# Kernel optimization log

Measured on AMD Instinct MI355X. Metric: run time of the kernel, lower is better.

The kernel has to match this reference:

```python
import jax, jax.numpy as jnp
import numpy as np
from jax.ops import segment_sum, segment_max

N_NODES = 50000
N_EDGES = 800000
B = 1024            # number of graphs
NODE_DIM = 21
ESM_DIM = 480
TAB_DIM = 7
H = 128             # hidden_dim
LSTM_H = H // 2     # 64 per direction
NEG_SLOPE = 0.2
BN_EPS = 1e-5


def setup_inputs() -> dict:
    key = jax.random.key(0)
    ks = iter(jax.random.split(key, 48))
    r = lambda shape, s=0.05: (s * jax.random.normal(next(ks), shape)).astype(jnp.float32)
    inp = {
        'x': jax.random.normal(next(ks), (N_NODES, NODE_DIM), dtype=jnp.float32),
        'edge_index': jax.random.randint(next(ks), (2, N_EDGES), 0, N_NODES, dtype=jnp.int64),
        'batch': jnp.sort(jax.random.randint(next(ks), (N_NODES,), 0, B, dtype=jnp.int64)),
        'esm_emb': jax.random.normal(next(ks), (B, ESM_DIM), dtype=jnp.float32),
        'tab_feats': jax.random.normal(next(ks), (B, TAB_DIM), dtype=jnp.float32),
        # GATConv 1 (heads=1)
        'gat1_W': r((H, NODE_DIM)), 'gat1_asrc': r((H,)), 'gat1_adst': r((H,)), 'gat1_b': r((H,)),
        # GATConv 2
        'gat2_W': r((H, H)), 'gat2_asrc': r((H,)), 'gat2_adst': r((H,)), 'gat2_b': r((H,)),
        # Bidirectional LSTM (seq_len=1, so a single cell step per direction)
        'lstm_Wih_f': r((4 * LSTM_H, ESM_DIM)), 'lstm_Whh_f': r((4 * LSTM_H, LSTM_H)),
        'lstm_bih_f': r((4 * LSTM_H,)), 'lstm_bhh_f': r((4 * LSTM_H,)),
        'lstm_Wih_r': r((4 * LSTM_H, ESM_DIM)), 'lstm_Whh_r': r((4 * LSTM_H, LSTM_H)),
        'lstm_bih_r': r((4 * LSTM_H,)), 'lstm_bhh_r': r((4 * LSTM_H,)),
        # tabular net
        'tab_W': r((64, TAB_DIM)), 'tab_b': r((64,)), 'tab_bn_g': jnp.ones((64,), jnp.float32), 'tab_bn_b': jnp.zeros((64,), jnp.float32),
        # fusion head
        'fus1_W': r((256, 320)), 'fus1_b': r((256,)), 'fus_bn_g': jnp.ones((256,), jnp.float32), 'fus_bn_b': jnp.zeros((256,), jnp.float32),
        'fus2_W': r((128, 256)), 'fus2_b': r((128,)),
        'fus3_W': r((1, 128)), 'fus3_b': r((1,)),
    }
    return inp


def _gat(h_in, src, dst, W, a_src, a_dst, bias):
    # PyG GATConv, heads=1, concat=True, self-loops already appended.
    h = h_in @ W.T                                  # [N, H]
    alpha_s = h @ a_src                             # [N]
    alpha_d = h @ a_dst                             # [N]
    e = jax.nn.leaky_relu(alpha_s[src] + alpha_d[dst], NEG_SLOPE)  # [E]
    m = segment_max(e, dst, num_segments=N_NODES)   # stable softmax per target
    ex = jnp.exp(e - m[dst])
    den = segment_sum(ex, dst, num_segments=N_NODES)
    coef = ex / (den[dst] + 1e-16)
    out = segment_sum(coef[:, None] * h[src], dst, num_segments=N_NODES)
    return out + bias


def _bn(x, g, b):
    # BatchNorm1d in training mode: biased batch statistics
    mu = jnp.mean(x, axis=0)
    var = jnp.var(x, axis=0)
    return (x - mu) * jax.lax.rsqrt(var + BN_EPS) * g + b


def _lstm_step(x, Wih, Whh, bih, bhh):
    # single step with zero initial (h, c); Whh term vanishes but kept for fidelity
    g = x @ Wih.T + bih + jnp.zeros((x.shape[0], Whh.shape[1]), x.dtype) @ Whh.T + bhh
    i, f, gg, o = jnp.split(g, 4, axis=1)           # PyTorch gate order i,f,g,o
    c = jax.nn.sigmoid(i) * jnp.tanh(gg)
    return jax.nn.sigmoid(o) * jnp.tanh(c)


def reference(x, edge_index, batch, esm_emb, tab_feats,
              gat1_W, gat1_asrc, gat1_adst, gat1_b,
              gat2_W, gat2_asrc, gat2_adst, gat2_b,
              lstm_Wih_f, lstm_Whh_f, lstm_bih_f, lstm_bhh_f,
              lstm_Wih_r, lstm_Whh_r, lstm_bih_r, lstm_bhh_r,
              tab_W, tab_b, tab_bn_g, tab_bn_b,
              fus1_W, fus1_b, fus_bn_g, fus_bn_b,
              fus2_W, fus2_b, fus3_W, fus3_b):
    sl = jnp.arange(N_NODES, dtype=edge_index.dtype)
    src = jnp.concatenate([edge_index[0], sl])      # add_self_loops=True default
    dst = jnp.concatenate([edge_index[1], sl])

    h1 = jax.nn.relu(_gat(x, src, dst, gat1_W, gat1_asrc, gat1_adst, gat1_b))
    h2 = jax.nn.relu(_gat(h1, src, dst, gat2_W, gat2_asrc, gat2_adst, gat2_b))

    counts = segment_sum(jnp.ones((N_NODES,), h2.dtype), batch, num_segments=B)
    graph_embed = segment_sum(h2, batch, num_segments=B) / jnp.maximum(counts, 1.0)[:, None]

    # bilstm over seq_len=1: output at last (only) step = concat(fwd, bwd)
    h_f = _lstm_step(esm_emb, lstm_Wih_f, lstm_Whh_f, lstm_bih_f, lstm_bhh_f)
    h_r = _lstm_step(esm_emb, lstm_Wih_r, lstm_Whh_r, lstm_bih_r, lstm_bhh_r)
    seq_embed = jnp.concatenate([h_f, h_r], axis=1)  # [B, 128]

    tab_embed = jax.nn.relu(_bn(tab_feats @ tab_W.T + tab_b, tab_bn_g, tab_bn_b))

    z = jnp.concatenate([graph_embed, seq_embed, tab_embed], axis=1)  # [B, 320]
    z = jax.nn.relu(_bn(z @ fus1_W.T + fus1_b, fus_bn_g, fus_bn_b))   # dropout: identity (eval)
    z = jax.nn.relu(z @ fus2_W.T + fus2_b)
    return z @ fus3_W.T + fus3_b                     # [B, 1]
```

## Files before the change

### kernel.cpp

```cpp
#include <hip/hip_runtime.h>
#include <hip/hip_bf16.h>

#define N_NODES 50000
#define N_PAD   50048
#define N_EDGES 800000
#define E_TOT   850000
#define NB      1024
#define ESM_DIM 480
#define HD      128
#define NBUCK   196
#define CAP     5120
#define EPB     3321
#define SC_BLK  256
#define CVT_BLK 256
#define BND_BLK 196
#define WC_BLK  16
#define TAB_BLK 4
#define G1B     782
#define LSTM_B  48
#define LG      384
#define AGG_GRID 12500
#define NL_BLK  512

typedef short short8 __attribute__((ext_vector_type(8)));
typedef unsigned short ushort8 __attribute__((ext_vector_type(8)));
typedef float f32x4 __attribute__((ext_vector_type(4)));

__device__ __forceinline__ float bf2f(unsigned int u) {
    union { unsigned int i; float f; } c; c.i = u << 16; return c.f;
}
__device__ __forceinline__ unsigned short f2bf(float f) {
    union { float f; unsigned int i; } c; c.f = f;
    unsigned int i = c.i;
    return (unsigned short)((i + 0x7FFFu + ((i >> 16) & 1u)) >> 16);
}
__device__ __forceinline__ void split2(float v, unsigned short& h, unsigned short& l) {
    h = f2bf(v);
    l = f2bf(v - bf2f(h));
}


__device__ void dev_scatter(const int* __restrict__ ei, int* __restrict__ gcur,
                            int* __restrict__ pairs, int blk) {
    __shared__ int hist[NBUCK];
    int t = threadIdx.x;
    for (int u = t; u < NBUCK; u += 256) hist[u] = 0;
    __syncthreads();
    int e0 = blk * EPB;
    int e1 = (e0 + EPB < E_TOT) ? e0 + EPB : E_TOT;
    for (int e = e0 + t; e < e1; e += 256) {
        int d = (e < N_EDGES) ? ei[N_EDGES + e] : (e - N_EDGES);
        atomicAdd(&hist[d >> 8], 1);
    }
    __syncthreads();
    for (int u = t; u < NBUCK; u += 256) {
        int c = hist[u];
        hist[u] = (c > 0) ? atomicAdd(&gcur[u], c) : 0;
    }
    __syncthreads();
    for (int e = e0 + t; e < e1; e += 256) {
        int s, d;
        if (e < N_EDGES) { s = ei[e]; d = ei[N_EDGES + e]; }
        else             { s = d = e - N_EDGES; }
        int bu = d >> 8;
        int pos = atomicAdd(&hist[bu], 1);
        pairs[bu * CAP + pos] = s | ((d & 255) << 16);
    }
}

__device__ void dev_cvt(const float* __restrict__ esm,
                        const float* __restrict__ Wf,
                        const float* __restrict__ Wr,
                        const float* __restrict__ W1,
                        unsigned short* __restrict__ esm_h, unsigned short* __restrict__ esm_l,
                        unsigned short* __restrict__ wg_h,  unsigned short* __restrict__ wg_l,
                        unsigned short* __restrict__ w1h,   unsigned short* __restrict__ w1l,
                        int blk) {
    int tid = blk * 256 + threadIdx.x;
    for (int u = tid; u < NB * 120; u += CVT_BLK * 256) {
        float4 v = ((const float4*)esm)[u];
        ushort4 h, l;
        split2(v.x, h.x, l.x); split2(v.y, h.y, l.y);
        split2(v.z, h.z, l.z); split2(v.w, h.w, l.w);
        ((ushort4*)esm_h)[u] = h; ((ushort4*)esm_l)[u] = l;
    }
    for (int u = tid; u < LG * 120; u += CVT_BLK * 256) {
        int n = u / 120, kk = u - n * 120;
        int rr = (n >= 192) ? n - 192 : n;
        const float* Ws = (n >= 192) ? Wr : Wf;
        int srow = (rr < 64) ? rr : rr + 64;
        float4 v = *(const float4*)&Ws[(size_t)srow * 480 + kk * 4];
        ushort4 h, l;
        split2(v.x, h.x, l.x); split2(v.y, h.y, l.y);
        split2(v.z, h.z, l.z); split2(v.w, h.w, l.w);
        ((ushort4*)wg_h)[u] = h; ((ushort4*)wg_l)[u] = l;
    }
    for (int u = tid; u < 128 * 32; u += CVT_BLK * 256) {
        int f = u >> 5, k = u & 31;
        float v = (k < 21) ? W1[f * 21 + k] : 0.f;
        unsigned short h, l;
        split2(v, h, l);
        w1h[u] = h; w1l[u] = l;
    }
}

__device__ void dev_tab4(const float* __restrict__ tf, const float* __restrict__ W,
                         const float* __restrict__ bias, const float* __restrict__ g,
                         const float* __restrict__ b, float* __restrict__ z, int blk) {
    __shared__ float ssum[16][16];
    __shared__ float ssq[16][16];
    int t = threadIdx.x;
    int rg = t >> 4, jl = t & 15;
    int j = blk * 16 + jl;
    float Wj[7];
#pragma unroll
    for (int k = 0; k < 7; ++k) Wj[k] = W[j * 7 + k];
    float bj = bias[j];
    float s = 0.f, q = 0.f;
    for (int rr = 0; rr < 64; ++rr) {
        int row = rg * 64 + rr;
        const float* xp = &tf[(size_t)row * 7];
        float a = bj;
#pragma unroll
        for (int k = 0; k < 7; ++k) a += xp[k] * Wj[k];
        s += a; q += a * a;
    }
    ssum[rg][jl] = s; ssq[rg][jl] = q;
    __syncthreads();
    for (int off = 8; off; off >>= 1) {
        if (rg < off) { ssum[rg][jl] += ssum[rg + off][jl]; ssq[rg][jl] += ssq[rg + off][jl]; }
        __syncthreads();
    }
    float mu = ssum[0][jl] * (1.f / 1024.f);
    float var = ssq[0][jl] * (1.f / 1024.f) - mu * mu;
    float sc = rsqrtf(var + 1e-5f) * g[j];
    float sh = b[j] - mu * sc;
    for (int rr = 0; rr < 64; ++rr) {
        int row = rg * 64 + rr;
        const float* xp = &tf[(size_t)row * 7];
        float a = bj;
#pragma unroll
        for (int k = 0; k < 7; ++k) a += xp[k] * Wj[k];
        z[(size_t)row * 320 + 256 + j] = fmaxf(a * sc + sh, 0.f);
    }
}

__global__ __launch_bounds__(256) void megaA(
        const int* __restrict__ ei, int* __restrict__ gcur, int* __restrict__ pairs,
        const float* __restrict__ esm, const float* __restrict__ Wih_f,
        const float* __restrict__ Wih_r, const float* __restrict__ gat1_W,
        unsigned short* __restrict__ esm_h, unsigned short* __restrict__ esm_l,
        unsigned short* __restrict__ wg_h,  unsigned short* __restrict__ wg_l,
        unsigned short* __restrict__ w1h,   unsigned short* __restrict__ w1l,
        const int* __restrict__ batch, int* __restrict__ gstart,
        const float* __restrict__ W2, unsigned short* __restrict__ Wb,
        const float* __restrict__ tf, const float* __restrict__ tab_W,
        const float* __restrict__ tab_b, const float* __restrict__ tab_g,
        const float* __restrict__ tab_bb, float* __restrict__ z) {
    int b = blockIdx.x, t = threadIdx.x;
    if (b < SC_BLK) {
        dev_scatter(ei, gcur, pairs, b);
    } else if (b < SC_BLK + CVT_BLK) {
        dev_cvt(esm, Wih_f, Wih_r, gat1_W, esm_h, esm_l, wg_h, wg_l, w1h, w1l, b - SC_BLK);
    } else if (b < SC_BLK + CVT_BLK + BND_BLK) {
        int i = (b - (SC_BLK + CVT_BLK)) * 256 + t;
        if (i >= N_NODES) return;
        int bb = batch[i];
        int bp = (i == 0) ? -1 : batch[i - 1];
        for (int g = bp + 1; g <= bb; ++g) gstart[g] = i;
        if (i == N_NODES - 1)
            for (int g = bb + 1; g <= NB; ++g) gstart[g] = N_NODES;
    } else if (b < SC_BLK + CVT_BLK + BND_BLK + WC_BLK) {
        int i = (b - (SC_BLK + CVT_BLK + BND_BLK)) * 256 + t;
        if (i >= 128 * 32) return;
        float4 v = ((const float4*)W2)[i];
        ((ushort4*)Wb)[i] = make_ushort4(f2bf(v.x), f2bf(v.y), f2bf(v.z), f2bf(v.w));
    } else {
        dev_tab4(tf, tab_W, tab_b, tab_g, tab_bb, z,
                 b - (SC_BLK + CVT_BLK + BND_BLK + WC_BLK));
    }
}


__device__ __forceinline__ float sigmoidf_(float x) { return 1.f / (1.f + __expf(-x)); }

__device__ void dev_gat1_mfma(const float* __restrict__ X,
                              const unsigned short* __restrict__ w1h,
                              const unsigned short* __restrict__ w1l,
                              const float* __restrict__ asrc, const float* __restrict__ adst,
                              unsigned short* __restrict__ out,
                              float* __restrict__ alpha_s, float* __restrict__ alpha_d,
                              int blk) {
    int t = threadIdx.x;
    int wid = t >> 6, L = t & 63, quad = L >> 4, lo = L & 15;
    int m0 = blk * 64 + wid * 16;
    int row = m0 + lo;
    const float* xr = X + (size_t)row * 21;
    int kbase = quad * 8;
    bool valid = row < N_NODES;
    float xv[8];
#pragma unroll
    for (int j = 0; j < 8; ++j) {
        int k = kbase + j;
        xv[j] = (valid && k < 21) ? xr[k] : 0.f;
    }
    short8 ah, al;
#pragma unroll
    for (int j = 0; j < 8; ++j) {
        unsigned short h, l;
        split2(xv[j], h, l);
        ah[j] = (short)h; al[j] = (short)l;
    }
    float as_p[4] = {0.f, 0.f, 0.f, 0.f};
    float ad_p[4] = {0.f, 0.f, 0.f, 0.f};
#pragma unroll
    for (int ft = 0; ft < 8; ++ft) {
        short8 bh = *(const short8*)&w1h[(ft * 16 + lo) * 32 + kbase];
        short8 bl = *(const short8*)&w1l[(ft * 16 + lo) * 32 + kbase];
        f32x4 acc = {0.f, 0.f, 0.f, 0.f};
        acc = __builtin_amdgcn_mfma_f32_16x16x32_bf16(ah, bh, acc, 0, 0, 0);
        acc = __builtin_amdgcn_mfma_f32_16x16x32_bf16(al, bh, acc, 0, 0, 0);
        acc = __builtin_amdgcn_mfma_f32_16x16x32_bf16(ah, bl, acc, 0, 0, 0);
        float asv = asrc[ft * 16 + lo];
        float adv = adst[ft * 16 + lo];
#pragma unroll
        for (int r = 0; r < 4; ++r) {
            int m = m0 + quad * 4 + r;
            out[(size_t)m * HD + ft * 16 + lo] = f2bf(acc[r]);
            as_p[r] += acc[r] * asv;
            ad_p[r] += acc[r] * adv;
        }
    }
#pragma unroll
    for (int off = 1; off < 16; off <<= 1) {
#pragma unroll
        for (int r = 0; r < 4; ++r) {
            as_p[r] += __shfl_xor(as_p[r], off);
            ad_p[r] += __shfl_xor(ad_p[r], off);
        }
    }
    if (lo == 0) {
#pragma unroll
        for (int r = 0; r < 4; ++r) {
            int m = m0 + quad * 4 + r;
            if (m < N_NODES) { alpha_s[m] = as_p[r]; alpha_d[m] = ad_p[r]; }
        }
    }
}

__device__ void dev_lstm_mfma(const unsigned short* __restrict__ Ah,
                              const unsigned short* __restrict__ Al,
                              const unsigned short* __restrict__ Bh,
                              const unsigned short* __restrict__ Bl,
                              float* __restrict__ G, int blk) {
    int t = threadIdx.x;
    int wid = t >> 6, L = t & 63, quad = L >> 4, lo = L & 15;
    int nt = blk % 3, mt = blk / 3;
    int m0 = mt * 64 + wid * 16;
    int n0 = nt * 128;
    f32x4 accs[8];
#pragma unroll
    for (int ft = 0; ft < 8; ++ft) accs[ft] = (f32x4){0.f, 0.f, 0.f, 0.f};
    const unsigned short* arh = Ah + (size_t)(m0 + lo) * ESM_DIM;
    const unsigned short* arl = Al + (size_t)(m0 + lo) * ESM_DIM;
    for (int k0 = 0; k0 < ESM_DIM; k0 += 32) {
        short8 ah = *(const short8*)&arh[k0 + quad * 8];
        short8 al = *(const short8*)&arl[k0 + quad * 8];
#pragma unroll
        for (int ft = 0; ft < 8; ++ft) {
            size_t boff = (size_t)(n0 + ft * 16 + lo) * ESM_DIM + k0 + quad * 8;
            short8 bh = *(const short8*)&Bh[boff];
            short8 bl = *(const short8*)&Bl[boff];
            accs[ft] = __builtin_amdgcn_mfma_f32_16x16x32_bf16(ah, bh, accs[ft], 0, 0, 0);
            accs[ft] = __builtin_amdgcn_mfma_f32_16x16x32_bf16(al, bh, accs[ft], 0, 0, 0);
            accs[ft] = __builtin_amdgcn_mfma_f32_16x16x32_bf16(ah, bl, accs[ft], 0, 0, 0);
        }
    }
#pragma unroll
    for (int ft = 0; ft < 8; ++ft) {
#pragma unroll
        for (int r = 0; r < 4; ++r)
            G[(size_t)(m0 + quad * 4 + r) * LG + n0 + ft * 16 + lo] = accs[ft][r];
    }
}

__global__ __launch_bounds__(256) void megaB(
        const int* __restrict__ gcur, const int* __restrict__ pairs,
        int* __restrict__ row_beg, int* __restrict__ row_end, int* __restrict__ csr_src,
        const float* __restrict__ x,
        const unsigned short* __restrict__ w1h, const unsigned short* __restrict__ w1l,
        const float* __restrict__ gat1_as, const float* __restrict__ gat1_ad,
        unsigned short* __restrict__ h0, float* __restrict__ alpha_s, float* __restrict__ alpha_d,
        const unsigned short* __restrict__ esm_h, const unsigned short* __restrict__ esm_l,
        const unsigned short* __restrict__ wg_h,  const unsigned short* __restrict__ wg_l,
        float* __restrict__ g_lstm) {
    int b = blockIdx.x, t = threadIdx.x;
    if (b < NBUCK) {
        __shared__ int dc[256];
        __shared__ int wt[4];
        __shared__ int cur[256];
        int rs = b * CAP;
        int re = rs + gcur[b];
        dc[t] = 0;
        __syncthreads();
        for (int i = rs + t; i < re; i += 256) atomicAdd(&dc[pairs[i] >> 16], 1);
        __syncthreads();
        int v = dc[t];
        int lane = t & 63, wid = t >> 6;
        int sc = v;
#pragma unroll
        for (int off = 1; off < 64; off <<= 1) {
            int n = __shfl_up(sc, off);
            if (lane >= off) sc += n;
        }
        if (lane == 63) wt[wid] = sc;
        __syncthreads();
        int pref = 0;
        for (int ww = 0; ww < wid; ++ww) pref += wt[ww];
        int beg = rs + pref + sc - v;
        int node = b * 256 + t;
        if (node < N_NODES) { row_beg[node] = beg; row_end[node] = beg + v; }
        cur[t] = beg;
        __syncthreads();
        for (int i = rs + t; i < re; i += 256) {
            int pk = pairs[i];
            int pos = atomicAdd(&cur[pk >> 16], 1);
            csr_src[pos] = pk & 0xFFFF;
        }
    } else if (b < NBUCK + LSTM_B) {
        dev_lstm_mfma(esm_h, esm_l, wg_h, wg_l, g_lstm, b - NBUCK);
    } else {
        dev_gat1_mfma(x, w1h, w1l, gat1_as, gat1_ad, h0, alpha_s, alpha_d,
                      b - (NBUCK + LSTM_B));
    }
}


__global__ __launch_bounds__(256) void gemm_mfma(const unsigned short* __restrict__ A,
                                                 const unsigned short* __restrict__ Wb,
                                                 const float* __restrict__ asrc,
                                                 const float* __restrict__ adst,
                                                 unsigned short* __restrict__ out,
                                                 float* __restrict__ alpha_s,
                                                 float* __restrict__ alpha_d, int M) {
    __shared__ unsigned short Wlds[128 * 136];
    int t = threadIdx.x;
    for (int u = t; u < 128 * 16; u += 256) {
        int row = u >> 4, seg = u & 15;
        *(ushort8*)&Wlds[row * 136 + seg * 8] = *(const ushort8*)&Wb[row * 128 + seg * 8];
    }
    __syncthreads();
    int wid = t >> 6, L = t & 63;
    int quad = L >> 4, lo = L & 15;
    int m0 = blockIdx.x * 64 + wid * 16;
    short8 afrag[4];
#pragma unroll
    for (int ch = 0; ch < 4; ++ch)
        afrag[ch] = *(const short8*)&A[(size_t)(m0 + lo) * HD + ch * 32 + quad * 8];
    float as_p[4] = {0.f, 0.f, 0.f, 0.f};
    float ad_p[4] = {0.f, 0.f, 0.f, 0.f};
#pragma unroll
    for (int ft = 0; ft < 8; ++ft) {
        f32x4 acc = {0.f, 0.f, 0.f, 0.f};
#pragma unroll
        for (int ch = 0; ch < 4; ++ch) {
            short8 b = *(const short8*)&Wlds[(ft * 16 + lo) * 136 + ch * 32 + quad * 8];
            acc = __builtin_amdgcn_mfma_f32_16x16x32_bf16(afrag[ch], b, acc, 0, 0, 0);
        }
        float asv = asrc[ft * 16 + lo];
        float adv = adst[ft * 16 + lo];
#pragma unroll
        for (int r = 0; r < 4; ++r) {
            int m = m0 + quad * 4 + r;
            if (m < M) out[(size_t)m * HD + ft * 16 + lo] = f2bf(acc[r]);
            as_p[r] += acc[r] * asv;
            ad_p[r] += acc[r] * adv;
        }
    }
#pragma unroll
    for (int off = 1; off < 16; off <<= 1) {
#pragma unroll
        for (int r = 0; r < 4; ++r) {
            as_p[r] += __shfl_xor(as_p[r], off);
            ad_p[r] += __shfl_xor(ad_p[r], off);
        }
    }
    if (lo == 0) {
#pragma unroll
        for (int r = 0; r < 4; ++r) {
            int m = m0 + quad * 4 + r;
            if (m < M) { alpha_s[m] = as_p[r]; alpha_d[m] = ad_p[r]; }
        }
    }
}


__global__ void gat_spmm(const unsigned short* __restrict__ h, const int* __restrict__ row_beg,
                         const int* __restrict__ row_end, const int* __restrict__ csr_src,
                         const float* __restrict__ alpha_s, const float* __restrict__ alpha_d,
                         const float* __restrict__ bias, unsigned short* __restrict__ outp,
                         const float* __restrict__ g_lstm,
                         const float* __restrict__ bihf, const float* __restrict__ bhhf,
                         const float* __restrict__ bihr, const float* __restrict__ bhhr,
                         float* __restrict__ z) {
    if (blockIdx.x >= AGG_GRID) {
        int idx = (blockIdx.x - AGG_GRID) * 256 + threadIdx.x;
        int bb = idx >> 7, jj = idx & 127;
        int dir = jj >> 6, j = jj & 63;
        const float* gb = g_lstm + (size_t)bb * LG + dir * 192;
        const float* bi = dir ? bihr : bihf;
        const float* bh = dir ? bhhr : bhhf;
        float gi = gb[j]        + bi[j]        + bh[j];
        float gg = gb[64 + j]   + bi[128 + j]  + bh[128 + j];
        float go = gb[128 + j]  + bi[192 + j]  + bh[192 + j];
        float c = sigmoidf_(gi) * tanhf(gg);
        z[(size_t)bb * 320 + 128 + jj] = sigmoidf_(go) * tanhf(c);
        return;
    }
    int w = (int)((blockIdx.x * (size_t)blockDim.x + threadIdx.x) >> 6);
    int lane = threadIdx.x & 63;
    if (w >= N_NODES) return;
    int grp = lane >> 4, l16 = lane & 15;
    int rs = row_beg[w], re = row_end[w];
    int deg = re - rs;
    float ad = alpha_d[w];
    float acc[8] = {0.f, 0.f, 0.f, 0.f, 0.f, 0.f, 0.f, 0.f};
    if (deg <= 64) {
        int s_reg = 0;
        float e = -1e30f;
        if (lane < deg) {
            s_reg = csr_src[rs + lane];
            float t0 = alpha_s[s_reg] + ad;
            e = (t0 > 0.f) ? t0 : 0.2f * t0;
        }
        float m = e;
#pragma unroll
        for (int off = 32; off; off >>= 1) m = fmaxf(m, __shfl_xor(m, off));
        float ex = (lane < deg) ? __expf(e - m) : 0.f;
        float den = ex;
#pragma unroll
        for (int off = 32; off; off >>= 1) den += __shfl_xor(den, off);
        float coef = ex / (den + 1e-16f);
        int i = rs + grp;
        for (; i + 4 < re; i += 8) {
            int idx = i - rs;
            float c0 = __shfl(coef, idx);
            int   s0 = __shfl(s_reg, idx);
            float c1 = __shfl(coef, idx + 4);
            int   s1 = __shfl(s_reg, idx + 4);
            ushort8 h0 = *(const ushort8*)&h[(size_t)s0 * HD + l16 * 8];
            ushort8 h1 = *(const ushort8*)&h[(size_t)s1 * HD + l16 * 8];
#pragma unroll
            for (int j = 0; j < 8; ++j) acc[j] += c0 * bf2f(h0[j]);
#pragma unroll
            for (int j = 0; j < 8; ++j) acc[j] += c1 * bf2f(h1[j]);
        }
        if (i < re) {
            int idx = i - rs;
            float c0 = __shfl(coef, idx);
            int   s0 = __shfl(s_reg, idx);
            ushort8 h0 = *(const ushort8*)&h[(size_t)s0 * HD + l16 * 8];
#pragma unroll
            for (int j = 0; j < 8; ++j) acc[j] += c0 * bf2f(h0[j]);
        }
    } else {
        float m = -1e30f;
        for (int i = rs + lane; i < re; i += 64) {
            int s = csr_src[i];
            float t0 = alpha_s[s] + ad;
            t0 = (t0 > 0.f) ? t0 : 0.2f * t0;
            m = fmaxf(m, t0);
        }
#pragma unroll
        for (int off = 32; off; off >>= 1) m = fmaxf(m, __shfl_xor(m, off));
        float den = 0.f;
        for (int i = rs + lane; i < re; i += 64) {
            int s = csr_src[i];
            float t0 = alpha_s[s] + ad;
            t0 = (t0 > 0.f) ? t0 : 0.2f * t0;
            den += __expf(t0 - m);
        }
#pragma unroll
        for (int off = 32; off; off >>= 1) den += __shfl_xor(den, off);
        float inv = 1.f / (den + 1e-16f);
        for (int i = rs + grp; i < re; i += 4) {
            int s = csr_src[i];
            float t0 = alpha_s[s] + ad;
            t0 = (t0 > 0.f) ? t0 : 0.2f * t0;
            float c = __expf(t0 - m) * inv;
            ushort8 hv = *(const ushort8*)&h[(size_t)s * HD + l16 * 8];
#pragma unroll
            for (int j = 0; j < 8; ++j) acc[j] += c * bf2f(hv[j]);
        }
    }
#pragma unroll
    for (int j = 0; j < 8; ++j) {
        acc[j] += __shfl_xor(acc[j], 16);
        acc[j] += __shfl_xor(acc[j], 32);
    }
    int f0 = l16 * 8 + grp * 2;
    float2 bv = *(const float2*)&bias[f0];
    float vx = fmaxf(acc[grp * 2]     + bv.x, 0.f);
    float vy = fmaxf(acc[grp * 2 + 1] + bv.y, 0.f);
    unsigned int pv = (unsigned int)f2bf(vx) | ((unsigned int)f2bf(vy) << 16);
    *(unsigned int*)&outp[(size_t)w * HD + f0] = pv;
}


__global__ void pool_kernel(const unsigned short* __restrict__ h, const int* __restrict__ start,
                            float* __restrict__ z) {
    int w = (int)((blockIdx.x * (size_t)blockDim.x + threadIdx.x) >> 6);
    int lane = threadIdx.x & 63;
    if (w >= NB) return;
    int grp = lane >> 4, l16 = lane & 15;
    int s0 = start[w], s1 = start[w + 1];
    float acc[8] = {0.f, 0.f, 0.f, 0.f, 0.f, 0.f, 0.f, 0.f};
    int n = s0 + grp;
    for (; n + 4 < s1; n += 8) {
        ushort8 a = *(const ushort8*)&h[(size_t)n * HD + l16 * 8];
        ushort8 b = *(const ushort8*)&h[(size_t)(n + 4) * HD + l16 * 8];
#pragma unroll
        for (int j = 0; j < 8; ++j) acc[j] += bf2f(a[j]);
#pragma unroll
        for (int j = 0; j < 8; ++j) acc[j] += bf2f(b[j]);
    }
    if (n < s1) {
        ushort8 a = *(const ushort8*)&h[(size_t)n * HD + l16 * 8];
#pragma unroll
        for (int j = 0; j < 8; ++j) acc[j] += bf2f(a[j]);
    }
#pragma unroll
    for (int j = 0; j < 8; ++j) {
        acc[j] += __shfl_xor(acc[j], 16);
        acc[j] += __shfl_xor(acc[j], 32);
    }
    float inv = 1.f / fmaxf((float)(s1 - s0), 1.f);
    int f0 = l16 * 8 + grp * 2;
    *(float2*)&z[(size_t)w * 320 + f0] =
        make_float2(acc[grp * 2] * inv, acc[grp * 2 + 1] * inv);
}


__global__ __launch_bounds__(256) void fus1_stats(const float* __restrict__ X,
                                                  const float* __restrict__ W1,
                                                  float* __restrict__ out,
                                                  float* __restrict__ colsum,
                                                  float* __restrict__ colsq) {
    __shared__ float Xs[16][33];
    __shared__ float Ws[64][33];
    __shared__ float cs[4][64];
    __shared__ float cq[4][64];
    int t = threadIdx.x;
    int r0 = blockIdx.x * 16;
    int fb = blockIdx.y * 64;
    const float* W = W1 + (size_t)fb * 320;
    int f = t & 63, rsub = t >> 6;
    float acc0 = 0.f, acc1 = 0.f, acc2 = 0.f, acc3 = 0.f;
    for (int kc = 0; kc < 320; kc += 32) {
        {
            int idx = t * 2, xr = idx >> 5, xk = idx & 31;
            const float2 v = *(const float2*)&X[(size_t)(r0 + xr) * 320 + kc + xk];
            Xs[xr][xk] = v.x; Xs[xr][xk + 1] = v.y;
        }
        {
            int wf = t >> 2, wk = (t & 3) * 8;
            const float4* p = (const float4*)&W[(size_t)wf * 320 + kc + wk];
            float4 a = p[0], b = p[1];
            Ws[wf][wk] = a.x; Ws[wf][wk + 1] = a.y; Ws[wf][wk + 2] = a.z; Ws[wf][wk + 3] = a.w;
            Ws[wf][wk + 4] = b.x; Ws[wf][wk + 5] = b.y; Ws[wf][wk + 6] = b.z; Ws[wf][wk + 7] = b.w;
        }
        __syncthreads();
#pragma unroll
        for (int k = 0; k < 32; ++k) {
            float w = Ws[f][k];
            acc0 += Xs[rsub][k] * w;
            acc1 += Xs[rsub + 4][k] * w;
            acc2 += Xs[rsub + 8][k] * w;
            acc3 += Xs[rsub + 12][k] * w;
        }
        __syncthreads();
    }
    out[(size_t)(r0 + rsub) * 256 + fb + f] = acc0;
    out[(size_t)(r0 + rsub + 4) * 256 + fb + f] = acc1;
    out[(size_t)(r0 + rsub + 8) * 256 + fb + f] = acc2;
    out[(size_t)(r0 + rsub + 12) * 256 + fb + f] = acc3;
    cs[rsub][f] = acc0 + acc1 + acc2 + acc3;
    cq[rsub][f] = acc0 * acc0 + acc1 * acc1 + acc2 * acc2 + acc3 * acc3;
    __syncthreads();
    if (rsub == 0) {
        atomicAdd(&colsum[fb + f], cs[0][f] + cs[1][f] + cs[2][f] + cs[3][f]);
        atomicAdd(&colsq[fb + f],  cq[0][f] + cq[1][f] + cq[2][f] + cq[3][f]);
    }
}


__global__ __launch_bounds__(256) void fus2_final(const float* __restrict__ z1pre,
                                                  const float* __restrict__ colsum,
                                                  const float* __restrict__ colsq,
                                                  const float* __restrict__ fus_g,
                                                  const float* __restrict__ fus_bb,
                                                  const float* __restrict__ W2,
                                                  const float* __restrict__ b2,
                                                  const float* __restrict__ W3,
                                                  const float* __restrict__ b3,
                                                  float* __restrict__ out) {
    __shared__ float Xs[16][33];
    __shared__ float Ws[128][33];
    __shared__ float rowsum[16];
    __shared__ float sc_[256], sh_[256];
    int t = threadIdx.x;
    {
        float mu = colsum[t] * (1.f / 1024.f);
        float var = colsq[t] * (1.f / 1024.f) - mu * mu;
        float s = rsqrtf(var + 1e-5f) * fus_g[t];
        sc_[t] = s;
        sh_[t] = fus_bb[t] - mu * s;
    }
    __syncthreads();
    int r0 = blockIdx.x * 16;
    int f = t & 127, rh = t >> 7;
    float acc[8] = {0.f, 0.f, 0.f, 0.f, 0.f, 0.f, 0.f, 0.f};
    for (int kc = 0; kc < 256; kc += 32) {
        {
            int idx = t * 2, xr = idx >> 5, xk = idx & 31;
            float2 v = *(const float2*)&z1pre[(size_t)(r0 + xr) * 256 + kc + xk];
            Xs[xr][xk]     = fmaxf(v.x * sc_[kc + xk]     + sh_[kc + xk], 0.f);
            Xs[xr][xk + 1] = fmaxf(v.y * sc_[kc + xk + 1] + sh_[kc + xk + 1], 0.f);
        }
#pragma unroll
        for (int i = 0; i < 4; ++i) {
            int id2 = t + 256 * i;
            int wf = id2 >> 3, wk = (id2 & 7) * 4;
            *(float4*)&Ws[wf][wk] = *(const float4*)&W2[(size_t)wf * 256 + kc + wk];
        }
        __syncthreads();
#pragma unroll
        for (int k = 0; k < 32; ++k) {
            float w = Ws[f][k];
#pragma unroll
            for (int r = 0; r < 8; ++r) acc[r] += Xs[rh * 8 + r][k] * w;
        }
        __syncthreads();
    }
    float bv = b2[f], wv = W3[f];
    if (t < 16) rowsum[t] = 0.f;
    __syncthreads();
#pragma unroll
    for (int r = 0; r < 8; ++r) {
        float v = fmaxf(acc[r] + bv, 0.f) * wv;
#pragma unroll
        for (int off = 32; off; off >>= 1) v += __shfl_xor(v, off);
        if ((t & 63) == 0) atomicAdd(&rowsum[rh * 8 + r], v);
    }
    __syncthreads();
    if (t < 16) out[r0 + t] = rowsum[t] + b3[0];
}


extern "C" void kernel_launch(void* const* d_in, const int* in_sizes, int n_in,
                              void* d_out, int out_size, void* d_ws, size_t ws_size,
                              hipStream_t stream) {
    const float* x        = (const float*)d_in[0];
    const int*   ei       = (const int*)d_in[1];
    const int*   batch    = (const int*)d_in[2];
    const float* esm      = (const float*)d_in[3];
    const float* tabf     = (const float*)d_in[4];
    const float* gat1_W   = (const float*)d_in[5];
    const float* gat1_as  = (const float*)d_in[6];
    const float* gat1_ad  = (const float*)d_in[7];
    const float* gat1_b   = (const float*)d_in[8];
    const float* gat2_W   = (const float*)d_in[9];
    const float* gat2_as  = (const float*)d_in[10];
    const float* gat2_ad  = (const float*)d_in[11];
    const float* gat2_b   = (const float*)d_in[12];
    const float* Wih_f    = (const float*)d_in[13];
    const float* bih_f    = (const float*)d_in[15];
    const float* bhh_f    = (const float*)d_in[16];
    const float* Wih_r    = (const float*)d_in[17];
    const float* bih_r    = (const float*)d_in[19];
    const float* bhh_r    = (const float*)d_in[20];
    const float* tab_W    = (const float*)d_in[21];
    const float* tab_b    = (const float*)d_in[22];
    const float* tab_g    = (const float*)d_in[23];
    const float* tab_bb   = (const float*)d_in[24];
    const float* fus1_W   = (const float*)d_in[25];
    const float* fus_g    = (const float*)d_in[27];
    const float* fus_bb   = (const float*)d_in[28];
    const float* fus2_W   = (const float*)d_in[29];
    const float* fus2_b   = (const float*)d_in[30];
    const float* fus3_W   = (const float*)d_in[31];
    const float* fus3_b   = (const float*)d_in[32];
    float* out = (float*)d_out;

    char* ws = (char*)d_ws;
    size_t off = 0;
    auto alloc = [&](size_t bytes) -> char* {
        char* p = ws + off;
        off += (bytes + 255) & ~(size_t)255;
        return p;
    };
    unsigned short* h0_bf = (unsigned short*)alloc((size_t)N_PAD * HD * 2);
    unsigned short* hA_bf = (unsigned short*)alloc((size_t)N_PAD * HD * 2);
    unsigned short* h2_bf = (unsigned short*)alloc((size_t)N_PAD * HD * 2);
    unsigned short* h_act = (unsigned short*)alloc((size_t)N_NODES * HD * 2);
    float* alpha_s = (float*)alloc((size_t)N_NODES * 4);
    float* alpha_d = (float*)alloc((size_t)N_NODES * 4);
    unsigned short* w2bf = (unsigned short*)alloc((size_t)HD * HD * 2);
    int*   row_beg = (int*)alloc((size_t)N_NODES * 4);
    int*   row_end = (int*)alloc((size_t)N_NODES * 4);
    int*   csr_src = (int*)alloc((size_t)NBUCK * CAP * 4);
    int*   pairs   = (int*)alloc((size_t)NBUCK * CAP * 4);
    int*   gstart  = (int*)alloc((size_t)(NB + 1) * 4);
    float* z1pre   = (float*)alloc((size_t)NB * 256 * 4);
    float* z       = (float*)alloc((size_t)NB * 320 * 4);
    float* g_lstm  = (float*)alloc((size_t)NB * LG * 4);
    unsigned short* esm_h = (unsigned short*)alloc((size_t)NB * ESM_DIM * 2);
    unsigned short* esm_l = (unsigned short*)alloc((size_t)NB * ESM_DIM * 2);
    unsigned short* wg_h  = (unsigned short*)alloc((size_t)LG * ESM_DIM * 2);
    unsigned short* wg_l  = (unsigned short*)alloc((size_t)LG * ESM_DIM * 2);
    unsigned short* w1h   = (unsigned short*)alloc((size_t)128 * 32 * 2);
    unsigned short* w1l   = (unsigned short*)alloc((size_t)128 * 32 * 2);
    int*   gcur    = (int*)alloc((size_t)NBUCK * 4);
    float* colsum  = (float*)alloc((size_t)256 * 4);
    float* colsq   = (float*)alloc((size_t)256 * 4);
    size_t zero_len = (size_t)((char*)colsq + 256 * 4 - (char*)gcur);
    hipMemsetAsync(gcur, 0, zero_len, stream);

    megaA<<<SC_BLK + CVT_BLK + BND_BLK + WC_BLK + TAB_BLK, 256, 0, stream>>>(
        ei, gcur, pairs, esm, Wih_f, Wih_r, gat1_W,
        esm_h, esm_l, wg_h, wg_l, w1h, w1l,
        batch, gstart, gat2_W, w2bf,
        tabf, tab_W, tab_b, tab_g, tab_bb, z);

    megaB<<<NBUCK + LSTM_B + G1B, 256, 0, stream>>>(
        gcur, pairs, row_beg, row_end, csr_src,
        x, w1h, w1l, gat1_as, gat1_ad, h0_bf, alpha_s, alpha_d,
        esm_h, esm_l, wg_h, wg_l, g_lstm);

    gat_spmm<<<AGG_GRID + NL_BLK, 256, 0, stream>>>(h0_bf, row_beg, row_end, csr_src,
                                                    alpha_s, alpha_d, gat1_b, hA_bf,
                                                    g_lstm, bih_f, bhh_f, bih_r, bhh_r, z);

    gemm_mfma<<<N_PAD / 64, 256, 0, stream>>>(hA_bf, w2bf, gat2_as, gat2_ad,
                                              h2_bf, alpha_s, alpha_d, N_NODES);

    gat_spmm<<<AGG_GRID, 256, 0, stream>>>(h2_bf, row_beg, row_end, csr_src,
                                           alpha_s, alpha_d, gat2_b, h_act,
                                           g_lstm, bih_f, bhh_f, bih_r, bhh_r, z);

    pool_kernel<<<(NB + 3) / 4, 256, 0, stream>>>(h_act, gstart, z);

    fus1_stats<<<dim3(64, 4), 256, 0, stream>>>(z, fus1_W, z1pre, colsum, colsq);

    fus2_final<<<64, 256, 0, stream>>>(z1pre, colsum, colsq, fus_g, fus_bb,
                                       fus2_W, fus2_b, fus3_W, fus3_b, out);

    (void)in_sizes; (void)n_in; (void)out_size; (void)ws_size;
}
```

Before: 332.3 us.

## Stage LSTM weights in LDS with finer N tiles and batch bucket pair loads

The LSTM gate GEMM inside megaB now uses 64-wide N tiles, which doubles its block count, and stages the hi/lo weight tiles in shared memory in K chunks of 96 so the four waves share them instead of each reading global memory. The CSR bucket build loops now load four pairs per thread per iteration before doing the LDS atomics, to raise memory-level parallelism. The cost is extra LDS use and barriers in the LSTM blocks, and more LSTM blocks competing with the other roles in the merged kernel.

```diff
diff --git a/kernel.cpp b/kernel.cpp
--- a/kernel.cpp
+++ b/kernel.cpp
@@ -17,7 +17,7 @@
 #define WC_BLK  16
 #define TAB_BLK 4
 #define G1B     782
-#define LSTM_B  48
+#define LSTM_B  96
 #define LG      384
 #define AGG_GRID 12500
 #define NL_BLK  512
@@ -253,31 +253,51 @@
                               const unsigned short* __restrict__ Bh,
                               const unsigned short* __restrict__ Bl,
                               float* __restrict__ G, int blk) {
+    __shared__ unsigned short Bsh[64][104];
+    __shared__ unsigned short Bsl[64][104];
     int t = threadIdx.x;
     int wid = t >> 6, L = t & 63, quad = L >> 4, lo = L & 15;
-    int nt = blk % 3, mt = blk / 3;
+    int nt = blk % 6, mt = blk / 6;
     int m0 = mt * 64 + wid * 16;
-    int n0 = nt * 128;
-    f32x4 accs[8];
-#pragma unroll
-    for (int ft = 0; ft < 8; ++ft) accs[ft] = (f32x4){0.f, 0.f, 0.f, 0.f};
+    int n0 = nt * 64;
+    f32x4 accs[4];
+#pragma unroll
+    for (int ft = 0; ft < 4; ++ft) accs[ft] = (f32x4){0.f, 0.f, 0.f, 0.f};
     const unsigned short* arh = Ah + (size_t)(m0 + lo) * ESM_DIM;
     const unsigned short* arl = Al + (size_t)(m0 + lo) * ESM_DIM;
-    for (int k0 = 0; k0 < ESM_DIM; k0 += 32) {
-        short8 ah = *(const short8*)&arh[k0 + quad * 8];
-        short8 al = *(const short8*)&arl[k0 + quad * 8];
-#pragma unroll
-        for (int ft = 0; ft < 8; ++ft) {
-            size_t boff = (size_t)(n0 + ft * 16 + lo) * ESM_DIM + k0 + quad * 8;
-            short8 bh = *(const short8*)&Bh[boff];
-            short8 bl = *(const short8*)&Bl[boff];
-            accs[ft] = __builtin_amdgcn_mfma_f32_16x16x32_bf16(ah, bh, accs[ft], 0, 0, 0);
-            accs[ft] = __builtin_amdgcn_mfma_f32_16x16x32_bf16(al, bh, accs[ft], 0, 0, 0);
-            accs[ft] = __builtin_amdgcn_mfma_f32_16x16x32_bf16(ah, bl, accs[ft], 0, 0, 0);
-        }
-    }
-#pragma unroll
-    for (int ft = 0; ft < 8; ++ft) {
+    for (int c = 0; c < 5; ++c) {
+        int k0c = c * 96;
+        short8 ah[3], al[3];
+#pragma unroll
+        for (int ks = 0; ks < 3; ++ks) {
+            ah[ks] = *(const short8*)&arh[k0c + ks * 32 + quad * 8];
+            al[ks] = *(const short8*)&arl[k0c + ks * 32 + quad * 8];
+        }
+#pragma unroll
+        for (int u = 0; u < 3; ++u) {
+            int li = u * 2048 + t * 8;
+            int row = li / 96, col = li % 96;
+            *(ushort8*)&Bsh[row][col] =
+                *(const ushort8*)&Bh[(size_t)(n0 + row) * ESM_DIM + k0c + col];
+            *(ushort8*)&Bsl[row][col] =
+                *(const ushort8*)&Bl[(size_t)(n0 + row) * ESM_DIM + k0c + col];
+        }
+        __syncthreads();
+#pragma unroll
+        for (int ks = 0; ks < 3; ++ks) {
+#pragma unroll
+            for (int ft = 0; ft < 4; ++ft) {
+                short8 bh = *(const short8*)&Bsh[ft * 16 + lo][ks * 32 + quad * 8];
+                short8 bl = *(const short8*)&Bsl[ft * 16 + lo][ks * 32 + quad * 8];
+                accs[ft] = __builtin_amdgcn_mfma_f32_16x16x32_bf16(ah[ks], bh, accs[ft], 0, 0, 0);
+                accs[ft] = __builtin_amdgcn_mfma_f32_16x16x32_bf16(al[ks], bh, accs[ft], 0, 0, 0);
+                accs[ft] = __builtin_amdgcn_mfma_f32_16x16x32_bf16(ah[ks], bl, accs[ft], 0, 0, 0);
+            }
+        }
+        __syncthreads();
+    }
+#pragma unroll
+    for (int ft = 0; ft < 4; ++ft) {
 #pragma unroll
         for (int r = 0; r < 4; ++r)
             G[(size_t)(m0 + quad * 4 + r) * LG + n0 + ft * 16 + lo] = accs[ft][r];
@@ -303,7 +323,17 @@
         int re = rs + gcur[b];
         dc[t] = 0;
         __syncthreads();
-        for (int i = rs + t; i < re; i += 256) atomicAdd(&dc[pairs[i] >> 16], 1);
+        for (int i = rs + t; i < re; i += 1024) {
+            int i1 = i + 256, i2 = i + 512, i3 = i + 768;
+            int p0 = pairs[i];
+            int p1 = (i1 < re) ? pairs[i1] : 0;
+            int p2 = (i2 < re) ? pairs[i2] : 0;
+            int p3 = (i3 < re) ? pairs[i3] : 0;
+            atomicAdd(&dc[p0 >> 16], 1);
+            if (i1 < re) atomicAdd(&dc[p1 >> 16], 1);
+            if (i2 < re) atomicAdd(&dc[p2 >> 16], 1);
+            if (i3 < re) atomicAdd(&dc[p3 >> 16], 1);
+        }
         __syncthreads();
         int v = dc[t];
         int lane = t & 63, wid = t >> 6;
@@ -322,10 +352,17 @@
         if (node < N_NODES) { row_beg[node] = beg; row_end[node] = beg + v; }
         cur[t] = beg;
         __syncthreads();
-        for (int i = rs + t; i < re; i += 256) {
-            int pk = pairs[i];
-            int pos = atomicAdd(&cur[pk >> 16], 1);
-            csr_src[pos] = pk & 0xFFFF;
+        for (int i = rs + t; i < re; i += 1024) {
+            int i1 = i + 256, i2 = i + 512, i3 = i + 768;
+            int p0 = pairs[i];
+            int p1 = (i1 < re) ? pairs[i1] : 0;
+            int p2 = (i2 < re) ? pairs[i2] : 0;
+            int p3 = (i3 < re) ? pairs[i3] : 0;
+            int pos0 = atomicAdd(&cur[p0 >> 16], 1);
+            csr_src[pos0] = p0 & 0xFFFF;
+            if (i1 < re) { int pos = atomicAdd(&cur[p1 >> 16], 1); csr_src[pos] = p1 & 0xFFFF; }
+            if (i2 < re) { int pos = atomicAdd(&cur[p2 >> 16], 1); csr_src[pos] = p2 & 0xFFFF; }
+            if (i3 < re) { int pos = atomicAdd(&cur[p3 >> 16], 1); csr_src[pos] = p3 & 0xFFFF; }
         }
     } else if (b < NBUCK + LSTM_B) {
         dev_lstm_mfma(esm_h, esm_l, wg_h, wg_l, g_lstm, b - NBUCK);
```

Measured after the change: 292.3 us. 12.1% less time.
